# Kernel tuning notes

Measured on AMD Instinct MI355X. Metric: run time of the kernel, lower is better.

The kernel has to match this reference:

```python
import jax, jax.numpy as jnp
import numpy as np

D_MODEL, D_K, D_V, H, D_FF = 512, 64, 64, 8, 2048
B, N = 8, 1024
LN_EPS = 1e-5


def _layer_norm(x, g, b):
    mu = jnp.mean(x, axis=-1, keepdims=True)
    var = jnp.mean((x - mu) ** 2, axis=-1, keepdims=True)
    return (x - mu) * jax.lax.rsqrt(var + LN_EPS) * g + b


def setup_inputs() -> dict:
    key = jax.random.key(0)
    ks = jax.random.split(key, 16)
    s = 0.02
    return {
        "queries": jax.random.normal(ks[0], (B, N, D_MODEL), jnp.float32),
        "keys": jax.random.normal(ks[1], (B, N, D_MODEL), jnp.float32),
        "values": jax.random.normal(ks[2], (B, N, D_MODEL), jnp.float32),
        "relative_geometry_weights": jax.random.uniform(ks[3], (B, H, N, N), jnp.float32),
        "pos": jax.random.normal(ks[4], (B, N, D_MODEL), jnp.float32),
        "Wq": jax.random.normal(ks[5], (D_MODEL, H * D_K), jnp.float32) * s,
        "bq": jnp.zeros((H * D_K,), jnp.float32),
        "Wk": jax.random.normal(ks[6], (D_MODEL, H * D_K), jnp.float32) * s,
        "bk": jnp.zeros((H * D_K,), jnp.float32),
        "Wv": jax.random.normal(ks[7], (D_MODEL, H * D_V), jnp.float32) * s,
        "bv": jnp.zeros((H * D_V,), jnp.float32),
        "Wo": jax.random.normal(ks[8], (H * D_V, D_MODEL), jnp.float32) * s,
        "bo": jnp.zeros((D_MODEL,), jnp.float32),
        "ln1_g": jnp.ones((D_MODEL,), jnp.float32),
        "ln1_b": jnp.zeros((D_MODEL,), jnp.float32),
        "W1": jax.random.normal(ks[9], (D_MODEL, D_FF), jnp.float32) * s,
        "b1": jnp.zeros((D_FF,), jnp.float32),
        "W2": jax.random.normal(ks[10], (D_FF, D_MODEL), jnp.float32) * s,
        "b2": jnp.zeros((D_MODEL,), jnp.float32),
        "ln2_g": jnp.ones((D_MODEL,), jnp.float32),
        "ln2_b": jnp.zeros((D_MODEL,), jnp.float32),
    }


def reference(queries, keys, values, relative_geometry_weights, pos,
              Wq, bq, Wk, bk, Wv, bv, Wo, bo, ln1_g, ln1_b,
              W1, b1, W2, b2, ln2_g, ln2_b):
    b, n, _ = queries.shape
    # positional injection on q/k only
    q_in = queries + pos
    k_in = keys + pos
    # projections -> [b, h, n, d]
    q = (q_in @ Wq + bq).reshape(b, n, H, D_K).transpose(0, 2, 1, 3)
    k = (k_in @ Wk + bk).reshape(b, n, H, D_K).transpose(0, 2, 1, 3)
    v = (values @ Wv + bv).reshape(b, n, H, D_V).transpose(0, 2, 1, 3)
    # scaled dot-product scores with geometry bias: log(clamp(w_g)) + scores
    att = jnp.einsum('bhqd,bhkd->bhqk', q, k) / jnp.sqrt(jnp.float32(D_K))
    w_mn = jnp.log(jnp.clip(relative_geometry_weights, 1e-6, None)) + att
    w_mn = jax.nn.softmax(w_mn, axis=-1)
    out = jnp.einsum('bhqk,bhkd->bhqd', w_mn, v)  # [b,h,n,d_v]
    out = out.transpose(0, 2, 1, 3).reshape(b, n, H * D_V) @ Wo + bo
    # residual + layernorm (dropout is identity in eval)
    att_out = _layer_norm(queries + out, ln1_g, ln1_b)
    # position-wise FFN with residual + layernorm
    ff = jax.nn.relu(att_out @ W1 + b1) @ W2 + b2
    return _layer_norm(att_out + ff, ln2_g, ln2_b)
```

## Files before the change

### kernel.cpp

```cpp
#include <hip/hip_runtime.h>
#include <hip/hip_bf16.h>
#include <stdint.h>

#define B_   8
#define N_   1024
#define DM   512
#define H_   8
#define DFF  2048
#define ROWS (B_ * N_)
#define QKV_LD (3 * DM)
#define LOG2E 1.4426950408889634f
#define SCL  (0.125f * LOG2E)

typedef __bf16 bf16x8 __attribute__((ext_vector_type(8)));
typedef float  f32x4  __attribute__((ext_vector_type(4)));

__device__ __forceinline__ void gld_lds16(const void* g, void* l) {
  __builtin_amdgcn_global_load_lds((__attribute__((address_space(1))) void*)g,
                                   (__attribute__((address_space(3))) void*)l, 16, 0, 0);
}

__device__ __forceinline__ unsigned short bfb(float x) {
  __bf16 h = (__bf16)x;
  unsigned short u;
  __builtin_memcpy(&u, &h, 2);
  return u;
}

__global__ __launch_bounds__(256) void prep_and_wt(
    const float* __restrict__ q, const float* __restrict__ k,
    const float* __restrict__ v, const float* __restrict__ pos,
    __bf16* __restrict__ xq, __bf16* __restrict__ xk, __bf16* __restrict__ xv,
    const float* __restrict__ Wq, const float* __restrict__ Wk,
    const float* __restrict__ Wv, const float* __restrict__ Wo,
    const float* __restrict__ W1, const float* __restrict__ W2,
    __bf16* __restrict__ WqkvT, __bf16* __restrict__ WoT,
    __bf16* __restrict__ W1T, __bf16* __restrict__ W2T) {
  __shared__ float tl[32][33];
  if (blockIdx.x < 4096) {
    int i = blockIdx.x * 256 + threadIdx.x;
    float4 pv = ((const float4*)pos)[i];
    float4 qv = ((const float4*)q)[i];
    float4 kv = ((const float4*)k)[i];
    float4 vv = ((const float4*)v)[i];
    ushort4 o;
    o.x = bfb(qv.x + pv.x); o.y = bfb(qv.y + pv.y); o.z = bfb(qv.z + pv.z); o.w = bfb(qv.w + pv.w);
    ((ushort4*)xq)[i] = o;
    o.x = bfb(kv.x + pv.x); o.y = bfb(kv.y + pv.y); o.z = bfb(kv.z + pv.z); o.w = bfb(kv.w + pv.w);
    ((ushort4*)xk)[i] = o;
    o.x = bfb(vv.x); o.y = bfb(vv.y); o.z = bfb(vv.z); o.w = bfb(vv.w);
    ((ushort4*)xv)[i] = o;
    return;
  }
  int idx = blockIdx.x - 4096;
  const float* src; __bf16* dst; int K, N, t;
  if (idx < 768) {
    src = idx < 256 ? Wq : (idx < 512 ? Wk : Wv);
    dst = WqkvT + (size_t)(idx >> 8) * 512 * 512;
    K = 512; N = 512; t = idx & 255;
  } else if (idx < 1024) { src = Wo; dst = WoT;  K = 512;  N = 512;  t = idx - 768; }
  else if (idx < 2048)   { src = W1; dst = W1T;  K = 512;  N = 2048; t = idx - 1024; }
  else                   { src = W2; dst = W2T;  K = 2048; N = 512;  t = idx - 2048; }
  int tiles_n = N >> 5;
  int tn = t & (tiles_n - 1), tk = t / tiles_n;
  int n0 = tn * 32, k0 = tk * 32;
  int x = threadIdx.x & 31, y4 = threadIdx.x >> 5;
  #pragma unroll
  for (int j = y4; j < 32; j += 8) tl[j][x] = src[(size_t)(k0 + j) * N + n0 + x];
  __syncthreads();
  #pragma unroll
  for (int j = y4; j < 32; j += 8)
    dst[(size_t)(n0 + j) * K + k0 + x] = (__bf16)tl[x][j];
}

template <int EPI, int BN>
__global__ __launch_bounds__(256, 2) void gemm_bt(
    const __bf16* __restrict__ A0, const __bf16* __restrict__ A1, const __bf16* __restrict__ A2,
    const __bf16* __restrict__ BT,
    const float* __restrict__ bias0, const float* __restrict__ bias1, const float* __restrict__ bias2,
    void* __restrict__ Cp, __bf16* __restrict__ Vtp, int M, int N, int K, int nsplit) {
  constexpr int NFR = BN / 32;
  constexpr int WCW = BN / 2;
  constexpr int BI  = BN / 32;
  __shared__ __align__(16) __bf16 As[2][128 * 64];
  __shared__ __align__(16) __bf16 Bs[2][BN * 64];
  int tid = threadIdx.x, lane = tid & 63;
  int wave = tid >> 6;
  int wr = (wave >> 1) * 64, wc = (wave & 1) * WCW;

  int gx = N / BN;
  int nwg = gridDim.x;
  int cpx = nwg >> 3;
  int swz = (blockIdx.x & 7) * cpx + (blockIdx.x >> 3);
  int bx = swz % gx, by = swz / gx;
  int row0 = by << 7, col0 = bx * BN;

  int asel = col0 / nsplit;
  const __bf16* A = asel == 0 ? A0 : (asel == 1 ? A1 : A2);
  const float* bias = asel == 0 ? bias0 : (asel == 1 ? bias1 : bias2);

  f32x4 acc[4][NFR] = {};

#define GSTAGE(BUF, KT)                                                        \
  { _Pragma("unroll")                                                          \
    for (int i = 0; i < 4; ++i) {                                              \
      int t = i * 256 + tid;                                                   \
      int r = t >> 3, cS = (t & 7) ^ (r & 7);                                  \
      gld_lds16(A + (size_t)(row0 + r) * K + (KT) + cS * 8, As[BUF] + t * 8);  \
    }                                                                          \
    _Pragma("unroll")                                                          \
    for (int i = 0; i < BI; ++i) {                                             \
      int t = i * 256 + tid;                                                   \
      int r = t >> 3, cS = (t & 7) ^ (r & 7);                                  \
      gld_lds16(BT + (size_t)(col0 + r) * K + (KT) + cS * 8, Bs[BUF] + t * 8); \
    } }

#define GCOMP(BUF)                                                             \
  { const __bf16* Asc = As[BUF];                                               \
    const __bf16* Bsc = Bs[BUF];                                               \
    _Pragma("unroll")                                                          \
    for (int ks = 0; ks < 2; ++ks) {                                           \
      bf16x8 af[4], bfr[NFR];                                                  \
      _Pragma("unroll")                                                        \
      for (int m = 0; m < 4; ++m) {                                            \
        int r = wr + m * 16 + (lane & 15);                                     \
        int c = (ks * 4 + (lane >> 4)) ^ (r & 7);                              \
        af[m] = *(const bf16x8*)(Asc + r * 64 + c * 8);                        \
      }                                                                        \
      _Pragma("unroll")                                                        \
      for (int n = 0; n < NFR; ++n) {                                          \
        int r = wc + n * 16 + (lane & 15);                                     \
        int c = (ks * 4 + (lane >> 4)) ^ (r & 7);                              \
        bfr[n] = *(const bf16x8*)(Bsc + r * 64 + c * 8);                       \
      }                                                                        \
      _Pragma("unroll")                                                        \
      for (int m = 0; m < 4; ++m)                                              \
        _Pragma("unroll")                                                      \
        for (int n = 0; n < NFR; ++n)                                          \
          acc[m][n] = __builtin_amdgcn_mfma_f32_16x16x32_bf16(af[m], bfr[n], acc[m][n], 0, 0, 0); \
    } }

  GSTAGE(0, 0)
  int cur = 0;
  for (int kt = 64; kt < K; kt += 64) {
    GSTAGE(cur ^ 1, kt)
    if constexpr (BN == 128) asm volatile("s_waitcnt vmcnt(8)" ::: "memory");
    else                     asm volatile("s_waitcnt vmcnt(6)" ::: "memory");
    __builtin_amdgcn_s_barrier();
    __builtin_amdgcn_sched_barrier(0);
    GCOMP(cur)
    __builtin_amdgcn_s_barrier();
    cur ^= 1;
  }
  asm volatile("s_waitcnt vmcnt(0)" ::: "memory");
  __builtin_amdgcn_s_barrier();
  __builtin_amdgcn_sched_barrier(0);
  GCOMP(cur)
#undef GSTAGE
#undef GCOMP

  int rb = row0 + wr + ((lane >> 4) << 2);
  int cb = col0 + wc + (lane & 15);
  if (EPI == 3 && asel == 2) {
    int bb = row0 >> 10;
    #pragma unroll
    for (int n = 0; n < NFR; ++n) {
      int c = cb + n * 16;
      int d = c & 63, hh = (c >> 6) & 7;
      float bv = bias[c % nsplit];
      size_t vbase = ((size_t)((bb * 8 + hh) * 64 + d)) << 10;
      #pragma unroll
      for (int m = 0; m < 4; ++m) {
        int r0 = (rb + m * 16) & 1023;
        ushort4 pk;
        pk.x = bfb(acc[m][n][0] + bv);
        pk.y = bfb(acc[m][n][1] + bv);
        pk.z = bfb(acc[m][n][2] + bv);
        pk.w = bfb(acc[m][n][3] + bv);
        *(ushort4*)((__bf16*)Vtp + vbase + r0) = pk;
      }
    }
    return;
  }
  #pragma unroll
  for (int n = 0; n < NFR; ++n) {
    int c = cb + n * 16;
    float bv = bias[c % nsplit];
    #pragma unroll
    for (int m = 0; m < 4; ++m) {
      #pragma unroll
      for (int j = 0; j < 4; ++j) {
        int r = rb + m * 16 + j;
        float v = acc[m][n][j] + bv;
        if (EPI == 1) v = fmaxf(v, 0.f);
        if (EPI == 2) ((float*)Cp)[(size_t)r * N + c] = v;
        else          ((__bf16*)Cp)[(size_t)r * N + c] = (__bf16)v;
      }
    }
  }
}

__global__ __launch_bounds__(256, 2) void attn_kernel(
    const __bf16* __restrict__ QKV, const __bf16* __restrict__ Vt,
    const float* __restrict__ rgw, __bf16* __restrict__ O) {
  __shared__ __align__(16) __bf16 Qs[64 * 64];
  __shared__ __align__(16) __bf16 Ks[2][64 * 64];
  __shared__ __align__(16) __bf16 Vs[2][64 * 64];
  __shared__ __align__(16) float  Ws[2][64 * 64];
  __shared__ __align__(16) __bf16 Ps[4][16 * 64];

  int tid = threadIdx.x, lane = tid & 63, wave = tid >> 6;
  int flat = (blockIdx.x & 7) * 128 + (blockIdx.x >> 3);
  int qt = flat & 15, h = (flat >> 4) & 7, b = flat >> 7;
  int q0 = qt * 64;
  const int g = lane >> 4, u = lane & 15;

  size_t wbase = ((size_t)(b * H_ + h) * N_ + (size_t)q0) * N_;

#define STAGE_T(BUF, KT)                                                       \
  {                                                                            \
    _Pragma("unroll")                                                          \
    for (int i = 0; i < 2; ++i) {                                              \
      int t = i * 256 + tid;                                                   \
      int r = t >> 3, cS = (t & 7) ^ (r & 7);                                  \
      gld_lds16(QKV + (size_t)(b * N_ + (KT) + r) * QKV_LD + DM + h * 64 + cS * 8, Ks[BUF] + t * 8); \
      gld_lds16(Vt + (size_t)((b * H_ + h) * 64 + r) * N_ + (KT) + cS * 8, Vs[BUF] + t * 8);         \
    }                                                                          \
    _Pragma("unroll")                                                          \
    for (int i = 0; i < 4; ++i) {                                              \
      int C = i * 256 + tid;                            \
      int R = C >> 4, c = C & 15;                                              \
      int sc = (c ^ (R & 7)) << 2;       \
      gld_lds16(rgw + wbase + (size_t)R * N_ + (KT) + sc, Ws[BUF] + C * 4);    \
    }                                                                          \
  }

  #pragma unroll
  for (int i = 0; i < 2; ++i) {
    int t = i * 256 + tid;
    int r = t >> 3, cS = (t & 7) ^ (r & 7);
    gld_lds16(QKV + (size_t)(b * N_ + q0 + r) * QKV_LD + h * 64 + cS * 8, Qs + t * 8);
  }
  STAGE_T(0, 0)

  float l = 0.f;
  f32x4 oacc[4] = {};
  bf16x8 qf[2];
  __bf16* pw = &Ps[wave][0];
  const int wrow = wave * 16 + u;
  union Pk { __bf16 h4[4]; unsigned long long q; };

#define PHASE(T16, DOSTAGE)                                                    \
  {                                                                            \
    asm volatile("s_waitcnt vmcnt(0)" ::: "memory");                           \
    __builtin_amdgcn_s_barrier();                                              \
    if (DOSTAGE) { STAGE_T(((T16) + 1) & 1, ((T16) + 1) * 64) }                \
    __builtin_amdgcn_sched_barrier(0);                                         \
    if ((T16) == 0) {                                                          \
      _Pragma("unroll")                                                        \
      for (int ks = 0; ks < 2; ++ks) {                                         \
        int c = (ks * 4 + g) ^ (wrow & 7);                                     \
        qf[ks] = *(const bf16x8*)(Qs + wrow * 64 + c * 8);                     \
      }                                                                        \
    }                                                                          \
    f32x4 s[4] = {};                                                           \
    __builtin_amdgcn_s_setprio(1);                                             \
    _Pragma("unroll")                                                          \
    for (int ks = 0; ks < 2; ++ks) {                                           \
      _Pragma("unroll")                                                        \
      for (int n = 0; n < 4; ++n) {                                            \
        int r = n * 16 + u;                                                    \
        int c = (ks * 4 + g) ^ (r & 7);                                        \
        bf16x8 kf = *(const bf16x8*)(Ks[(T16) & 1] + r * 64 + c * 8);          \
        s[n] = __builtin_amdgcn_mfma_f32_16x16x32_bf16(kf, qf[ks], s[n], 0, 0, 0); \
      }                                                                        \
    }                                                                          \
    __builtin_amdgcn_s_setprio(0);                                             \
                        \
    f32x4 w[4];                                                                \
    _Pragma("unroll")                                                          \
    for (int n = 0; n < 4; ++n)                                                \
      w[n] = *(const f32x4*)(Ws[(T16) & 1] + wrow * 64 + (((4 * n + g) ^ (u & 7)) << 2)); \
    _Pragma("unroll")                                                          \
    for (int n = 0; n < 4; ++n) {                                              \
      Pk pk;                                                                   \
      _Pragma("unroll")                                                        \
      for (int j = 0; j < 4; ++j) {                                            \
        float pv = fmaxf(w[n][j], 1e-6f) * exp2f(s[n][j] * SCL);               \
        l += pv;                                                               \
        pk.h4[j] = (__bf16)pv;                                                 \
      }                                                                        \
      int bcol = 2 * n + (g >> 1);                                             \
      *(unsigned long long*)(pw + u * 64 + ((bcol ^ (u & 7)) << 3) + ((g & 1) << 2)) = pk.q; \
    }                                                                          \
    __builtin_amdgcn_s_setprio(1);                                             \
    _Pragma("unroll")                                                          \
    for (int ks = 0; ks < 2; ++ks) {                                           \
      int cp = (ks * 4 + g) ^ (u & 7);                                         \
      bf16x8 pa = *(const bf16x8*)(pw + u * 64 + cp * 8);                      \
      _Pragma("unroll")                                                        \
      for (int n = 0; n < 4; ++n) {                                            \
        int r = n * 16 + u;                                                    \
        int c = (ks * 4 + g) ^ (r & 7);                                        \
        bf16x8 vb = *(const bf16x8*)(Vs[(T16) & 1] + r * 64 + c * 8);          \
        oacc[n] = __builtin_amdgcn_mfma_f32_16x16x32_bf16(pa, vb, oacc[n], 0, 0, 0); \
      }                                                                        \
    }                                                                          \
    __builtin_amdgcn_s_setprio(0);                                             \
  }

  PHASE(0, 1)  PHASE(1, 1)  PHASE(2, 1)  PHASE(3, 1)
  PHASE(4, 1)  PHASE(5, 1)  PHASE(6, 1)  PHASE(7, 1)
  PHASE(8, 1)  PHASE(9, 1)  PHASE(10, 1) PHASE(11, 1)
  PHASE(12, 1) PHASE(13, 1) PHASE(14, 1) PHASE(15, 0)
#undef PHASE
#undef STAGE_T

  l += __shfl_xor(l, 16);
  l += __shfl_xor(l, 32);
  float linv[4];
  #pragma unroll
  for (int j = 0; j < 4; ++j)
    linv[j] = 1.f / __shfl(l, (lane & 48) | (g * 4 + j));

  int orow = b * N_ + q0 + wave * 16 + g * 4;
  int ocol = h * 64 + u;
  #pragma unroll
  for (int j = 0; j < 4; ++j)
    #pragma unroll
    for (int n = 0; n < 4; ++n)
      O[(size_t)(orow + j) * DM + ocol + n * 16] = (__bf16)(oacc[n][j] * linv[j]);
}

template <int WRITE_BF, int X2BF>
__global__ __launch_bounds__(256) void ln_kernel(
    const float* __restrict__ x1, const void* __restrict__ x2v,
    const float* __restrict__ gw, const float* __restrict__ bw,
    float* __restrict__ outf, __bf16* __restrict__ outb) {
  __shared__ float red[8];
  int row = blockIdx.x, t = threadIdx.x;
  size_t base = (size_t)row * DM;
  float2 a = ((const float2*)(x1 + base))[t];
  float b0, b1;
  if (X2BF) {
    unsigned p = ((const unsigned*)x2v)[base / 2 + t];
    union { unsigned u; float f; } c0, c1;
    c0.u = p << 16; c1.u = p & 0xffff0000u;
    b0 = c0.f; b1 = c1.f;
  } else {
    float2 bb = ((const float2*)x2v)[base / 2 + t];
    b0 = bb.x; b1 = bb.y;
  }
  float v0 = a.x + b0, v1 = a.y + b1;
  float s = v0 + v1, s2 = v0 * v0 + v1 * v1;
  #pragma unroll
  for (int o = 32; o; o >>= 1) { s += __shfl_xor(s, o); s2 += __shfl_xor(s2, o); }
  int wave = t >> 6;
  if ((t & 63) == 0) { red[wave] = s; red[4 + wave] = s2; }
  __syncthreads();
  s = red[0] + red[1] + red[2] + red[3];
  s2 = red[4] + red[5] + red[6] + red[7];
  float mu = s * (1.f / DM);
  float var = s2 * (1.f / DM) - mu * mu;
  float rstd = rsqrtf(var + 1e-5f);
  float y0 = (v0 - mu) * rstd * gw[2 * t] + bw[2 * t];
  float y1 = (v1 - mu) * rstd * gw[2 * t + 1] + bw[2 * t + 1];
  float2 r; r.x = y0; r.y = y1;
  ((float2*)(outf + base))[t] = r;
  if (WRITE_BF) {
    ushort2 h; h.x = bfb(y0); h.y = bfb(y1);
    ((ushort2*)(outb + base))[t] = h;
  }
}

extern "C" void kernel_launch(void* const* d_in, const int* in_sizes, int n_in,
                              void* d_out, int out_size, void* d_ws, size_t ws_size,
                              hipStream_t stream) {
  const float* queries = (const float*)d_in[0];
  const float* keys    = (const float*)d_in[1];
  const float* values  = (const float*)d_in[2];
  const float* rgw     = (const float*)d_in[3];
  const float* pos     = (const float*)d_in[4];
  const float* Wq = (const float*)d_in[5];
  const float* bq = (const float*)d_in[6];
  const float* Wk = (const float*)d_in[7];
  const float* bk = (const float*)d_in[8];
  const float* Wv = (const float*)d_in[9];
  const float* bv = (const float*)d_in[10];
  const float* Wo = (const float*)d_in[11];
  const float* bo = (const float*)d_in[12];
  const float* ln1g = (const float*)d_in[13];
  const float* ln1b = (const float*)d_in[14];
  const float* W1 = (const float*)d_in[15];
  const float* b1 = (const float*)d_in[16];
  const float* W2 = (const float*)d_in[17];
  const float* b2 = (const float*)d_in[18];
  const float* ln2g = (const float*)d_in[19];
  const float* ln2b = (const float*)d_in[20];
  float* out = (float*)d_out;

  char* ws = (char*)d_ws;
  const size_t SZX = (size_t)ROWS * DM * 2;
  __bf16* Xq    = (__bf16*)(ws);
  __bf16* Xk    = (__bf16*)(ws + SZX);
  __bf16* Xv    = (__bf16*)(ws + 2 * SZX);
  __bf16* WqkvT = (__bf16*)(ws + 3 * SZX);
  __bf16* WoT   = (__bf16*)(ws + 3 * SZX + 1572864);
  __bf16* W1T   = (__bf16*)(ws + 3 * SZX + 2097152);
  __bf16* W2T   = (__bf16*)(ws + 3 * SZX + 4194304);
  __bf16* QKV   = (__bf16*)(ws + 3 * SZX + 6291456);
  __bf16* Vt    = (__bf16*)(ws + 3 * SZX + 6291456 + 3 * SZX);
  __bf16* Oat   = (__bf16*)(ws + 3 * SZX + 6291456 + 4 * SZX);
  __bf16* attprojb = Xq;
  __bf16* attoutb  = Xv;
  float*  attoutf  = (float*)QKV;
  __bf16* ff2b     = Vt;
  __bf16* ff1      = (__bf16*)(ws + 3 * SZX + 6291456 + 5 * SZX);

  prep_and_wt<<<4096 + 3072, 256, 0, stream>>>(
      queries, keys, values, pos, Xq, Xk, Xv,
      Wq, Wk, Wv, Wo, W1, W2, WqkvT, WoT, W1T, W2T);

  gemm_bt<3, 128><<<(ROWS / 128) * (QKV_LD / 128), 256, 0, stream>>>(
      Xq, Xk, Xv, WqkvT, bq, bk, bv, QKV, Vt, ROWS, QKV_LD, DM, DM);

  attn_kernel<<<B_ * H_ * (N_ / 64), 256, 0, stream>>>(QKV, Vt, rgw, Oat);

  gemm_bt<0, 64><<<(ROWS / 128) * (DM / 64), 256, 0, stream>>>(
      Oat, Oat, Oat, WoT, bo, bo, bo, attprojb, nullptr, ROWS, DM, DM, DM);

  ln_kernel<1, 1><<<ROWS, 256, 0, stream>>>(queries, attprojb, ln1g, ln1b, attoutf, attoutb);

  gemm_bt<1, 128><<<(ROWS / 128) * (DFF / 128), 256, 0, stream>>>(
      attoutb, attoutb, attoutb, W1T, b1, b1, b1, ff1, nullptr, ROWS, DFF, DM, DFF);

  gemm_bt<0, 64><<<(ROWS / 128) * (DM / 64), 256, 0, stream>>>(
      ff1, ff1, ff1, W2T, b2, b2, b2, ff2b, nullptr, ROWS, DM, DFF, DM);

  ln_kernel<0, 1><<<ROWS, 256, 0, stream>>>(attoutf, ff2b, ln2g, ln2b, out, nullptr);
}
```

Baseline: 223.9 us.

## Double attention query tile to 128 rows with 8 waves sharing K/V tiles

```diff
diff --git a/kernel.cpp b/kernel.cpp
--- a/kernel.cpp
+++ b/kernel.cpp
@@ -200,44 +200,46 @@
   }
 }
 
-__global__ __launch_bounds__(256, 2) void attn_kernel(
+__global__ __launch_bounds__(512, 2) void attn_kernel(
     const __bf16* __restrict__ QKV, const __bf16* __restrict__ Vt,
     const float* __restrict__ rgw, __bf16* __restrict__ O) {
-  __shared__ __align__(16) __bf16 Qs[64 * 64];
+  __shared__ __align__(16) __bf16 Qs[128 * 64];
   __shared__ __align__(16) __bf16 Ks[2][64 * 64];
   __shared__ __align__(16) __bf16 Vs[2][64 * 64];
-  __shared__ __align__(16) float  Ws[2][64 * 64];
-  __shared__ __align__(16) __bf16 Ps[4][16 * 64];
+  __shared__ __align__(16) float  Ws[2][2][64 * 64];
+  __shared__ __align__(16) __bf16 Ps[8][16 * 64];
 
   int tid = threadIdx.x, lane = tid & 63, wave = tid >> 6;
-  int flat = (blockIdx.x & 7) * 128 + (blockIdx.x >> 3);
-  int qt = flat & 15, h = (flat >> 4) & 7, b = flat >> 7;
-  int q0 = qt * 64;
+  int flat = (blockIdx.x & 7) * 64 + (blockIdx.x >> 3);
+  int qt = flat & 7, h = (flat >> 3) & 7, b = flat >> 6;
+  int q0 = qt * 128;
   const int g = lane >> 4, u = lane & 15;
+  const int tau = wave >> 2;
+  const int sr  = (wave & 3) * 16;
+  const int wrow = sr + u;
 
   size_t wbase = ((size_t)(b * H_ + h) * N_ + (size_t)q0) * N_;
 
 #define STAGE_T(BUF, KT)                                                       \
   {                                                                            \
-    _Pragma("unroll")                                                          \
-    for (int i = 0; i < 2; ++i) {                                              \
-      int t = i * 256 + tid;                                                   \
-      int r = t >> 3, cS = (t & 7) ^ (r & 7);                                  \
-      gld_lds16(QKV + (size_t)(b * N_ + (KT) + r) * QKV_LD + DM + h * 64 + cS * 8, Ks[BUF] + t * 8); \
-      gld_lds16(Vt + (size_t)((b * H_ + h) * 64 + r) * N_ + (KT) + cS * 8, Vs[BUF] + t * 8);         \
-    }                                                                          \
+    { int r = tid >> 3, cS = (tid & 7) ^ (r & 7);                              \
+      gld_lds16(QKV + (size_t)(b * N_ + (KT) + r) * QKV_LD + DM + h * 64 + cS * 8, Ks[BUF] + tid * 8); \
+      gld_lds16(Vt + (size_t)((b * H_ + h) * 64 + r) * N_ + (KT) + cS * 8, Vs[BUF] + tid * 8); }      \
     _Pragma("unroll")                                                          \
     for (int i = 0; i < 4; ++i) {                                              \
-      int C = i * 256 + tid;                            \
-      int R = C >> 4, c = C & 15;                                              \
+      int C = i * 512 + tid;                            \
+      int tt = C >> 10;                                     \
+      int Ci = C & 1023;                                                       \
+      int R = Ci >> 4, c = Ci & 15;                                            \
       int sc = (c ^ (R & 7)) << 2;       \
-      gld_lds16(rgw + wbase + (size_t)R * N_ + (KT) + sc, Ws[BUF] + C * 4);    \
+      gld_lds16(rgw + wbase + (size_t)(tt * 64 + R) * N_ + (KT) + sc,          \
+                Ws[BUF][tt] + Ci * 4);                                         \
     }                                                                          \
   }
 
   #pragma unroll
   for (int i = 0; i < 2; ++i) {
-    int t = i * 256 + tid;
+    int t = i * 512 + tid;
     int r = t >> 3, cS = (t & 7) ^ (r & 7);
     gld_lds16(QKV + (size_t)(b * N_ + q0 + r) * QKV_LD + h * 64 + cS * 8, Qs + t * 8);
   }
@@ -247,7 +249,7 @@
   f32x4 oacc[4] = {};
   bf16x8 qf[2];
   __bf16* pw = &Ps[wave][0];
-  const int wrow = wave * 16 + u;
+  const int qrow = tau * 64 + wrow;
   union Pk { __bf16 h4[4]; unsigned long long q; };
 
 #define PHASE(T16, DOSTAGE)                                                    \
@@ -259,8 +261,8 @@
     if ((T16) == 0) {                                                          \
       _Pragma("unroll")                                                        \
       for (int ks = 0; ks < 2; ++ks) {                                         \
-        int c = (ks * 4 + g) ^ (wrow & 7);                                     \
-        qf[ks] = *(const bf16x8*)(Qs + wrow * 64 + c * 8);                     \
+        int c = (ks * 4 + g) ^ (qrow & 7);                                     \
+        qf[ks] = *(const bf16x8*)(Qs + qrow * 64 + c * 8);                     \
       }                                                                        \
     }                                                                          \
     f32x4 s[4] = {};                                                           \
@@ -280,7 +282,7 @@
     f32x4 w[4];                                                                \
     _Pragma("unroll")                                                          \
     for (int n = 0; n < 4; ++n)                                                \
-      w[n] = *(const f32x4*)(Ws[(T16) & 1] + wrow * 64 + (((4 * n + g) ^ (u & 7)) << 2)); \
+      w[n] = *(const f32x4*)(Ws[(T16) & 1][tau] + wrow * 64 + (((4 * n + g) ^ (u & 7)) << 2)); \
     _Pragma("unroll")                                                          \
     for (int n = 0; n < 4; ++n) {                                              \
       Pk pk;                                                                   \
@@ -323,7 +325,7 @@
   for (int j = 0; j < 4; ++j)
     linv[j] = 1.f / __shfl(l, (lane & 48) | (g * 4 + j));
 
-  int orow = b * N_ + q0 + wave * 16 + g * 4;
+  int orow = b * N_ + q0 + tau * 64 + sr + g * 4;
   int ocol = h * 64 + u;
   #pragma unroll
   for (int j = 0; j < 4; ++j)
@@ -424,7 +426,7 @@
   gemm_bt<3, 128><<<(ROWS / 128) * (QKV_LD / 128), 256, 0, stream>>>(
       Xq, Xk, Xv, WqkvT, bq, bk, bv, QKV, Vt, ROWS, QKV_LD, DM, DM);
 
-  attn_kernel<<<B_ * H_ * (N_ / 64), 256, 0, stream>>>(QKV, Vt, rgw, Oat);
+  attn_kernel<<<B_ * H_ * (N_ / 128), 512, 0, stream>>>(QKV, Vt, rgw, Oat);
 
   gemm_bt<0, 64><<<(ROWS / 128) * (DM / 64), 256, 0, stream>>>(
       Oat, Oat, Oat, WoT, bo, bo, bo, attprojb, nullptr, ROWS, DM, DM, DM);
```

New measurement: 229.0 us. 2.3% more time.

## Stream geometry weights directly into registers and shrink attention LDS for higher occupancy

Applied to the files above, without the earlier changes.

```diff
diff --git a/kernel.cpp b/kernel.cpp
--- a/kernel.cpp
+++ b/kernel.cpp
@@ -200,14 +200,12 @@
   }
 }
 
-__global__ __launch_bounds__(256, 2) void attn_kernel(
+__global__ __launch_bounds__(256, 4) void attn_kernel(
     const __bf16* __restrict__ QKV, const __bf16* __restrict__ Vt,
     const float* __restrict__ rgw, __bf16* __restrict__ O) {
-  __shared__ __align__(16) __bf16 Qs[64 * 64];
+  __shared__ __align__(16) __bf16 QsPs[64 * 64];
   __shared__ __align__(16) __bf16 Ks[2][64 * 64];
   __shared__ __align__(16) __bf16 Vs[2][64 * 64];
-  __shared__ __align__(16) float  Ws[2][64 * 64];
-  __shared__ __align__(16) __bf16 Ps[4][16 * 64];
 
   int tid = threadIdx.x, lane = tid & 63, wave = tid >> 6;
   int flat = (blockIdx.x & 7) * 128 + (blockIdx.x >> 3);
@@ -215,9 +213,10 @@
   int q0 = qt * 64;
   const int g = lane >> 4, u = lane & 15;
 
-  size_t wbase = ((size_t)(b * H_ + h) * N_ + (size_t)q0) * N_;
-
-#define STAGE_T(BUF, KT)                                                       \
+  const float* rgw_p = rgw +
+      ((size_t)(b * H_ + h) * N_ + (size_t)(q0 + wave * 16 + u)) * N_ + g * 4;
+
+#define STAGE_KV(BUF, KT)                                                      \
   {                                                                            \
     _Pragma("unroll")                                                          \
     for (int i = 0; i < 2; ++i) {                                              \
@@ -226,41 +225,44 @@
       gld_lds16(QKV + (size_t)(b * N_ + (KT) + r) * QKV_LD + DM + h * 64 + cS * 8, Ks[BUF] + t * 8); \
       gld_lds16(Vt + (size_t)((b * H_ + h) * 64 + r) * N_ + (KT) + cS * 8, Vs[BUF] + t * 8);         \
     }                                                                          \
-    _Pragma("unroll")                                                          \
-    for (int i = 0; i < 4; ++i) {                                              \
-      int C = i * 256 + tid;                            \
-      int R = C >> 4, c = C & 15;                                              \
-      int sc = (c ^ (R & 7)) << 2;       \
-      gld_lds16(rgw + wbase + (size_t)R * N_ + (KT) + sc, Ws[BUF] + C * 4);    \
-    }                                                                          \
+  }
+#define RPF(W, T)                                                              \
+  {                                                                            \
+    _Pragma("unroll")                                                          \
+    for (int n = 0; n < 4; ++n)                                                \
+      W[n] = __builtin_nontemporal_load((const f32x4*)(rgw_p + (size_t)(T) * 64 + n * 16)); \
   }
 
   #pragma unroll
   for (int i = 0; i < 2; ++i) {
     int t = i * 256 + tid;
     int r = t >> 3, cS = (t & 7) ^ (r & 7);
-    gld_lds16(QKV + (size_t)(b * N_ + q0 + r) * QKV_LD + h * 64 + cS * 8, Qs + t * 8);
-  }
-  STAGE_T(0, 0)
+    gld_lds16(QKV + (size_t)(b * N_ + q0 + r) * QKV_LD + h * 64 + cS * 8, QsPs + t * 8);
+  }
+  STAGE_KV(0, 0)
+  __builtin_amdgcn_sched_barrier(0);
+  f32x4 wA[4], wB[4];
+  RPF(wA, 0) RPF(wB, 1)
+  __builtin_amdgcn_sched_barrier(0);
 
   float l = 0.f;
   f32x4 oacc[4] = {};
   bf16x8 qf[2];
-  __bf16* pw = &Ps[wave][0];
+  __bf16* pw = &QsPs[wave * 16 * 64];
   const int wrow = wave * 16 + u;
   union Pk { __bf16 h4[4]; unsigned long long q; };
 
-#define PHASE(T16, DOSTAGE)                                                    \
+#define PHASE(T16, WAITSTR, DOSTAGE, DORPF, WCON)                              \
   {                                                                            \
-    asm volatile("s_waitcnt vmcnt(0)" ::: "memory");                           \
+    asm volatile(WAITSTR ::: "memory");                                        \
     __builtin_amdgcn_s_barrier();                                              \
-    if (DOSTAGE) { STAGE_T(((T16) + 1) & 1, ((T16) + 1) * 64) }                \
+    if (DOSTAGE) { STAGE_KV(((T16) + 1) & 1, ((T16) + 1) * 64) }               \
     __builtin_amdgcn_sched_barrier(0);                                         \
     if ((T16) == 0) {                                                          \
       _Pragma("unroll")                                                        \
       for (int ks = 0; ks < 2; ++ks) {                                         \
         int c = (ks * 4 + g) ^ (wrow & 7);                                     \
-        qf[ks] = *(const bf16x8*)(Qs + wrow * 64 + c * 8);                     \
+        qf[ks] = *(const bf16x8*)(QsPs + wrow * 64 + c * 8);                   \
       }                                                                        \
     }                                                                          \
     f32x4 s[4] = {};                                                           \
@@ -276,23 +278,22 @@
       }                                                                        \
     }                                                                          \
     __builtin_amdgcn_s_setprio(0);                                             \
-                        \
-    f32x4 w[4];                                                                \
-    _Pragma("unroll")                                                          \
-    for (int n = 0; n < 4; ++n)                                                \
-      w[n] = *(const f32x4*)(Ws[(T16) & 1] + wrow * 64 + (((4 * n + g) ^ (u & 7)) << 2)); \
+    if ((T16) == 0) __builtin_amdgcn_s_barrier();   \
     _Pragma("unroll")                                                          \
     for (int n = 0; n < 4; ++n) {                                              \
       Pk pk;                                                                   \
       _Pragma("unroll")                                                        \
       for (int j = 0; j < 4; ++j) {                                            \
-        float pv = fmaxf(w[n][j], 1e-6f) * exp2f(s[n][j] * SCL);               \
+        float pv = fmaxf(WCON[n][j], 1e-6f) * exp2f(s[n][j] * SCL);            \
         l += pv;                                                               \
         pk.h4[j] = (__bf16)pv;                                                 \
       }                                                                        \
       int bcol = 2 * n + (g >> 1);                                             \
       *(unsigned long long*)(pw + u * 64 + ((bcol ^ (u & 7)) << 3) + ((g & 1) << 2)) = pk.q; \
     }                                                                          \
+    __builtin_amdgcn_sched_barrier(0);                                         \
+    if (DORPF) { RPF(WCON, (T16) + 2) }                                        \
+    __builtin_amdgcn_sched_barrier(0);                                         \
     __builtin_amdgcn_s_setprio(1);                                             \
     _Pragma("unroll")                                                          \
     for (int ks = 0; ks < 2; ++ks) {                                           \
@@ -309,12 +310,25 @@
     __builtin_amdgcn_s_setprio(0);                                             \
   }
 
-  PHASE(0, 1)  PHASE(1, 1)  PHASE(2, 1)  PHASE(3, 1)
-  PHASE(4, 1)  PHASE(5, 1)  PHASE(6, 1)  PHASE(7, 1)
-  PHASE(8, 1)  PHASE(9, 1)  PHASE(10, 1) PHASE(11, 1)
-  PHASE(12, 1) PHASE(13, 1) PHASE(14, 1) PHASE(15, 0)
+  PHASE(0,  "s_waitcnt vmcnt(8)", 1, 1, wA)
+  PHASE(1,  "s_waitcnt vmcnt(4)", 1, 1, wB)
+  PHASE(2,  "s_waitcnt vmcnt(4)", 1, 1, wA)
+  PHASE(3,  "s_waitcnt vmcnt(4)", 1, 1, wB)
+  PHASE(4,  "s_waitcnt vmcnt(4)", 1, 1, wA)
+  PHASE(5,  "s_waitcnt vmcnt(4)", 1, 1, wB)
+  PHASE(6,  "s_waitcnt vmcnt(4)", 1, 1, wA)
+  PHASE(7,  "s_waitcnt vmcnt(4)", 1, 1, wB)
+  PHASE(8,  "s_waitcnt vmcnt(4)", 1, 1, wA)
+  PHASE(9,  "s_waitcnt vmcnt(4)", 1, 1, wB)
+  PHASE(10, "s_waitcnt vmcnt(4)", 1, 1, wA)
+  PHASE(11, "s_waitcnt vmcnt(4)", 1, 1, wB)
+  PHASE(12, "s_waitcnt vmcnt(4)", 1, 1, wA)
+  PHASE(13, "s_waitcnt vmcnt(4)", 1, 1, wB)
+  PHASE(14, "s_waitcnt vmcnt(4)", 1, 0, wA)
+  PHASE(15, "s_waitcnt vmcnt(0)", 0, 0, wB)
 #undef PHASE
-#undef STAGE_T
+#undef STAGE_KV
+#undef RPF
 
   l += __shfl_xor(l, 16);
   l += __shfl_xor(l, 32);
```

Measured after the change: 209.8 us, median of 3. -6.3%, faster.

## Triple-buffer geometry weights and prefetch two tiles ahead in attention

Applied to the files above, without the earlier changes.

```diff
diff --git a/kernel.cpp b/kernel.cpp
--- a/kernel.cpp
+++ b/kernel.cpp
@@ -203,21 +203,20 @@
 __global__ __launch_bounds__(256, 2) void attn_kernel(
     const __bf16* __restrict__ QKV, const __bf16* __restrict__ Vt,
     const float* __restrict__ rgw, __bf16* __restrict__ O) {
-  __shared__ __align__(16) __bf16 Qs[64 * 64];
   __shared__ __align__(16) __bf16 Ks[2][64 * 64];
   __shared__ __align__(16) __bf16 Vs[2][64 * 64];
-  __shared__ __align__(16) float  Ws[2][64 * 64];
-  __shared__ __align__(16) __bf16 Ps[4][16 * 64];
+  __shared__ __align__(16) float  Ws[3][64 * 64];
 
   int tid = threadIdx.x, lane = tid & 63, wave = tid >> 6;
   int flat = (blockIdx.x & 7) * 128 + (blockIdx.x >> 3);
   int qt = flat & 15, h = (flat >> 4) & 7, b = flat >> 7;
   int q0 = qt * 64;
   const int g = lane >> 4, u = lane & 15;
+  const int wrow = wave * 16 + u;
 
   size_t wbase = ((size_t)(b * H_ + h) * N_ + (size_t)q0) * N_;
 
-#define STAGE_T(BUF, KT)                                                       \
+#define STAGE_KV(BUF, KT)                                                      \
   {                                                                            \
     _Pragma("unroll")                                                          \
     for (int i = 0; i < 2; ++i) {                                              \
@@ -226,43 +225,55 @@
       gld_lds16(QKV + (size_t)(b * N_ + (KT) + r) * QKV_LD + DM + h * 64 + cS * 8, Ks[BUF] + t * 8); \
       gld_lds16(Vt + (size_t)((b * H_ + h) * 64 + r) * N_ + (KT) + cS * 8, Vs[BUF] + t * 8);         \
     }                                                                          \
+  }
+#define STAGE_W(BUF3, KT)                                                      \
+  {                                                                            \
     _Pragma("unroll")                                                          \
     for (int i = 0; i < 4; ++i) {                                              \
       int C = i * 256 + tid;                            \
       int R = C >> 4, c = C & 15;                                              \
-      int sc = (c ^ (R & 7)) << 2;       \
-      gld_lds16(rgw + wbase + (size_t)R * N_ + (KT) + sc, Ws[BUF] + C * 4);    \
-    }                                                                          \
-  }
-
-  #pragma unroll
-  for (int i = 0; i < 2; ++i) {
-    int t = i * 256 + tid;
-    int r = t >> 3, cS = (t & 7) ^ (r & 7);
-    gld_lds16(QKV + (size_t)(b * N_ + q0 + r) * QKV_LD + h * 64 + cS * 8, Qs + t * 8);
-  }
-  STAGE_T(0, 0)
+      int sc = (c ^ (R & 7)) << 2;                                             \
+      gld_lds16(rgw + wbase + (size_t)R * N_ + (KT) + sc, Ws[BUF3] + C * 4);   \
+    }                                                                          \
+  }
+
+  {
+    __bf16* QsA = (__bf16*)Ws[2];
+    #pragma unroll
+    for (int i = 0; i < 2; ++i) {
+      int t = i * 256 + tid;
+      int r = t >> 3, cS = (t & 7) ^ (r & 7);
+      gld_lds16(QKV + (size_t)(b * N_ + q0 + r) * QKV_LD + h * 64 + cS * 8, QsA + t * 8);
+    }
+  }
+  STAGE_KV(0, 0)
+  STAGE_W(0, 0)
+  __builtin_amdgcn_sched_barrier(0);
+  STAGE_W(1, 64)
+  __builtin_amdgcn_sched_barrier(0);
 
   float l = 0.f;
   f32x4 oacc[4] = {};
   bf16x8 qf[2];
-  __bf16* pw = &Ps[wave][0];
-  const int wrow = wave * 16 + u;
   union Pk { __bf16 h4[4]; unsigned long long q; };
 
-#define PHASE(T16, DOSTAGE)                                                    \
+#define PHASE(T16, WAITSTR, DOKV, DOW)                                         \
   {                                                                            \
-    asm volatile("s_waitcnt vmcnt(0)" ::: "memory");                           \
+    asm volatile(WAITSTR ::: "memory");                                        \
     __builtin_amdgcn_s_barrier();                                              \
-    if (DOSTAGE) { STAGE_T(((T16) + 1) & 1, ((T16) + 1) * 64) }                \
-    __builtin_amdgcn_sched_barrier(0);                                         \
     if ((T16) == 0) {                                                          \
+      const __bf16* QsA = (const __bf16*)Ws[2];                                \
       _Pragma("unroll")                                                        \
       for (int ks = 0; ks < 2; ++ks) {                                         \
         int c = (ks * 4 + g) ^ (wrow & 7);                                     \
-        qf[ks] = *(const bf16x8*)(Qs + wrow * 64 + c * 8);                     \
-      }                                                                        \
-    }                                                                          \
+        qf[ks] = *(const bf16x8*)(QsA + wrow * 64 + c * 8);                    \
+      }                                                                        \
+      __syncthreads();        \
+    }                                                                          \
+    if (DOKV) { STAGE_KV(((T16) + 1) & 1, ((T16) + 1) * 64) }                  \
+    __builtin_amdgcn_sched_barrier(0);                                         \
+    if (DOW) { STAGE_W(((T16) + 2) % 3, ((T16) + 2) * 64) }                    \
+    __builtin_amdgcn_sched_barrier(0);                                         \
     f32x4 s[4] = {};                                                           \
     __builtin_amdgcn_s_setprio(1);                                             \
     _Pragma("unroll")                                                          \
@@ -276,11 +287,15 @@
       }                                                                        \
     }                                                                          \
     __builtin_amdgcn_s_setprio(0);                                             \
-                        \
+     \
+     \
+    float* wsb = Ws[(T16) % 3];                                                \
     f32x4 w[4];                                                                \
     _Pragma("unroll")                                                          \
     for (int n = 0; n < 4; ++n)                                                \
-      w[n] = *(const f32x4*)(Ws[(T16) & 1] + wrow * 64 + (((4 * n + g) ^ (u & 7)) << 2)); \
+      w[n] = *(const f32x4*)(wsb + wrow * 64 + (((4 * n + g) ^ (u & 7)) << 2)); \
+    __builtin_amdgcn_sched_barrier(0);   \
+    __bf16* pw = (__bf16*)(wsb + wave * 16 * 64);                              \
     _Pragma("unroll")                                                          \
     for (int n = 0; n < 4; ++n) {                                              \
       Pk pk;                                                                   \
@@ -309,12 +324,25 @@
     __builtin_amdgcn_s_setprio(0);                                             \
   }
 
-  PHASE(0, 1)  PHASE(1, 1)  PHASE(2, 1)  PHASE(3, 1)
-  PHASE(4, 1)  PHASE(5, 1)  PHASE(6, 1)  PHASE(7, 1)
-  PHASE(8, 1)  PHASE(9, 1)  PHASE(10, 1) PHASE(11, 1)
-  PHASE(12, 1) PHASE(13, 1) PHASE(14, 1) PHASE(15, 0)
+  PHASE(0,  "s_waitcnt vmcnt(4)", 1, 1)
+  PHASE(1,  "s_waitcnt vmcnt(4)", 1, 1)
+  PHASE(2,  "s_waitcnt vmcnt(4)", 1, 1)
+  PHASE(3,  "s_waitcnt vmcnt(4)", 1, 1)
+  PHASE(4,  "s_waitcnt vmcnt(4)", 1, 1)
+  PHASE(5,  "s_waitcnt vmcnt(4)", 1, 1)
+  PHASE(6,  "s_waitcnt vmcnt(4)", 1, 1)
+  PHASE(7,  "s_waitcnt vmcnt(4)", 1, 1)
+  PHASE(8,  "s_waitcnt vmcnt(4)", 1, 1)
+  PHASE(9,  "s_waitcnt vmcnt(4)", 1, 1)
+  PHASE(10, "s_waitcnt vmcnt(4)", 1, 1)
+  PHASE(11, "s_waitcnt vmcnt(4)", 1, 1)
+  PHASE(12, "s_waitcnt vmcnt(4)", 1, 1)
+  PHASE(13, "s_waitcnt vmcnt(4)", 1, 1)
+  PHASE(14, "s_waitcnt vmcnt(4)", 1, 0)
+  PHASE(15, "s_waitcnt vmcnt(0)", 0, 0)
 #undef PHASE
-#undef STAGE_T
+#undef STAGE_KV
+#undef STAGE_W
 
   l += __shfl_xor(l, 16);
   l += __shfl_xor(l, 32);
```

Result: no change. 225.4 us (+0.7%).
